# Kernel optimization log

Hardware: AMD Instinct MI355X
Metric: run time of the kernel (lower is better)

## Reference

```python
import jax, jax.numpy as jnp
import numpy as np

B, NPG, K_DYN, H, C = 8, 4096, 8, 2, 64   # graphs, nodes/graph, kNN, heads, head dim
N = B * NPG
E = 524288
CAP = 20.0
NEG = 0.2


def _leaky(x):
    return jax.nn.leaky_relu(x, NEG)


def _bn(x, g, b):
    # BatchNorm1d, training-mode statistics over the node dim (biased var, eps=1e-5)
    m = jnp.mean(x, 0)
    v = jnp.mean((x - m) ** 2, 0)
    return (x - m) * jax.lax.rsqrt(v + 1e-5) * g + b


def _gatv2(x, src, dst, wl, bl, wr, br, att, bias, ea=None, we=None):
    # PyG GATv2Conv, heads=H, concat=False (mean over heads), dropout in eval mode
    n = x.shape[0]
    xl = (x @ wl + bl).reshape(n, H, C)   # source transform
    xr = (x @ wr + br).reshape(n, H, C)   # target transform
    e = xl[src] + xr[dst]                 # [E,H,C]
    if ea is not None:
        e = e + (ea @ we).reshape(-1, H, C)
    e = _leaky(e)
    logit = jnp.sum(e * att, -1)          # [E,H]
    m = jax.ops.segment_max(logit, dst, num_segments=n)
    m = jnp.where(jnp.isfinite(m), m, 0.0)
    ex = jnp.exp(logit - m[dst])
    den = jax.ops.segment_sum(ex, dst, num_segments=n) + 1e-16
    alpha = ex / den[dst]                 # segment softmax over incoming edges
    out = jax.ops.segment_sum(alpha[..., None] * xl[src], dst, num_segments=n)
    return jnp.mean(out, 1) + bias        # concat=False -> mean over heads


def _dyn_agg(h, w1, b1, w2, b2):
    # dynamic kNN in feature space (per graph, detached), gather-MLP-mean aggregation
    h3 = h.reshape(B, NPG, -1)
    hd = jax.lax.stop_gradient(h3)
    sq = jnp.sum(hd * hd, -1)
    d = sq[:, :, None] + sq[:, None, :] - 2.0 * jnp.einsum('bnd,bmd->bnm', hd, hd)
    d = jnp.where(jnp.eye(NPG, dtype=bool), jnp.inf, d)  # exclude self
    _, idx = jax.lax.top_k(-d, K_DYN)                    # [B,n,K] nearest neighbors
    hn = jax.vmap(lambda hb, ib: hb[ib])(h3, idx)        # [B,n,K,D]
    hi = jnp.broadcast_to(h3[:, :, None, :], hn.shape)
    msg = jnp.concatenate([hi, hn - hi], -1)             # cat([h[row], h[col]-h[row]])
    msg = _leaky(msg @ w1 + b1) @ w2 + b2
    # every node emits exactly K edges -> scatter_add/count == mean over K
    return jnp.mean(msg, 2).reshape(N, -1)


def setup_inputs():
    key = jax.random.key(0)
    ks = iter(jax.random.split(key, 64))
    def rn(shape, scale=1.0):
        return jax.random.normal(next(ks), shape, dtype=jnp.float32) * scale
    hd = 64
    return {
        'x': rn((N, 5)),
        'edge_attr': rn((E, 6)),
        'edge_index': jax.random.randint(next(ks), (2, E), 0, N, dtype=jnp.int32),
        'g1_wl': rn((5, H * C), 0.3), 'g1_bl': rn((H * C,), 0.02),
        'g1_wr': rn((5, H * C), 0.3), 'g1_br': rn((H * C,), 0.02),
        'g1_we': rn((6, H * C), 0.3),
        'g1_att': rn((H, C), 0.1), 'g1_bias': rn((C,), 0.02),
        'bn1_g': jnp.ones((hd,), jnp.float32), 'bn1_b': jnp.zeros((hd,), jnp.float32),
        'em_w1': rn((2 * hd, hd), 0.08), 'em_b1': rn((hd,), 0.02),
        'em_w2': rn((hd, hd), 0.12), 'em_b2': rn((hd,), 0.02),
        'bn2_g': jnp.ones((hd,), jnp.float32), 'bn2_b': jnp.zeros((hd,), jnp.float32),
        'g2_wl': rn((hd, H * C), 0.12), 'g2_bl': rn((H * C,), 0.02),
        'g2_wr': rn((hd, H * C), 0.12), 'g2_br': rn((H * C,), 0.02),
        'g2_att': rn((H, C), 0.1), 'g2_bias': rn((C,), 0.02),
        'bn3_g': jnp.ones((hd,), jnp.float32), 'bn3_b': jnp.zeros((hd,), jnp.float32),
        'gate_w1': rn((hd, hd), 0.12), 'gate_b1': rn((hd,), 0.02),
        'gate_w2': rn((hd, 1), 0.12), 'gate_b2': rn((1,), 0.02),
        'ctx_w1': rn((hd, hd), 0.12), 'ctx_b1': rn((hd,), 0.02),
        'ctx_w2': rn((hd, hd), 0.12), 'ctx_b2': rn((hd,), 0.02),
        'dec_w1': rn((hd + hd + 5, 128), 0.09), 'dec_b1': rn((128,), 0.02),
        'ln_g': jnp.ones((128,), jnp.float32), 'ln_b': jnp.zeros((128,), jnp.float32),
        'dec_w2': rn((128, 64), 0.09), 'dec_b2': rn((64,), 0.02),
        'dec_w3': rn((64, 3), 0.12), 'dec_b3': rn((3,), 0.02),
    }


def reference(x, edge_attr, edge_index, g1_wl, g1_bl, g1_wr, g1_br, g1_we, g1_att, g1_bias,
              bn1_g, bn1_b, em_w1, em_b1, em_w2, em_b2, bn2_g, bn2_b,
              g2_wl, g2_bl, g2_wr, g2_br, g2_att, g2_bias, bn3_g, bn3_b,
              gate_w1, gate_b1, gate_w2, gate_b2, ctx_w1, ctx_b1, ctx_w2, ctx_b2,
              dec_w1, dec_b1, ln_g, ln_b, dec_w2, dec_b2, dec_w3, dec_b3):
    src, dst = edge_index[0], edge_index[1]
    h = _leaky(_bn(_gatv2(x, src, dst, g1_wl, g1_bl, g1_wr, g1_br, g1_att, g1_bias, edge_attr, g1_we), bn1_g, bn1_b))
    h = _leaky(_bn(_dyn_agg(h, em_w1, em_b1, em_w2, em_b2), bn2_g, bn2_b))
    h = _leaky(_bn(_gatv2(h, src, dst, g2_wl, g2_bl, g2_wr, g2_br, g2_att, g2_bias), bn3_g, bn3_b))
    # attentional pooling per graph (equal-sized graphs -> reshape instead of segment ops)
    h3 = h.reshape(B, NPG, -1)
    gate = jnp.tanh(h3 @ gate_w1 + gate_b1) @ gate_w2 + gate_b2   # [B,n,1]
    alpha = jax.nn.softmax(gate, axis=1)
    g = jnp.sum(alpha * h3, 1)                                    # [B,hd]
    g = _leaky(g @ ctx_w1 + ctx_b1) @ ctx_w2 + ctx_b2
    gfull = jnp.broadcast_to(g[:, None, :], (B, NPG, g.shape[-1])).reshape(N, -1)
    hf = jnp.concatenate([h, gfull, x], 1)                        # [N,133]
    d1 = _leaky(hf @ dec_w1 + dec_b1)
    mu = jnp.mean(d1, -1, keepdims=True)
    var = jnp.mean((d1 - mu) ** 2, -1, keepdims=True)
    d1 = (d1 - mu) * jax.lax.rsqrt(var + 1e-5) * ln_g + ln_b       # LayerNorm(128)
    d2 = _leaky(d1 @ dec_w2 + dec_b2)
    out3 = d2 @ dec_w3 + dec_b3
    return x[:, :3] + jnp.tanh(out3) * CAP
```

## Files before the change

### kernel.cpp

```cpp
#include <hip/hip_runtime.h>

#define NN   32768
#define NPG  4096
#define NGR  8
#define NE   524288
#define NEGS 0.2f

typedef float  v4f __attribute__((ext_vector_type(4)));
typedef short  v8s __attribute__((ext_vector_type(8)));

__device__ __forceinline__ float lrelu(float x){ return x > 0.f ? x : NEGS*x; }

__device__ __forceinline__ unsigned short f2bf(float v){
  unsigned int u = __float_as_uint(v);
  u = u + 0x7fffu + ((u >> 16) & 1u);
  return (unsigned short)(u >> 16);
}
__device__ __forceinline__ float bf2f(unsigned short s){
  return __uint_as_float(((unsigned int)s) << 16);
}

__global__ __launch_bounds__(256) void k_xform5(
    const float* __restrict__ x,
    const float* __restrict__ wl, const float* __restrict__ bl,
    const float* __restrict__ wr, const float* __restrict__ br,
    float* __restrict__ xl, float* __restrict__ xr) {
  int t = blockIdx.x * 256 + threadIdx.x;
  int n = t >> 7, oc = t & 127;
  const float* xp = x + n * 5;
  float a = bl[oc], b = br[oc];
  #pragma unroll
  for (int j = 0; j < 5; ++j) {
    float v = xp[j];
    a += v * wl[j * 128 + oc];
    b += v * wr[j * 128 + oc];
  }
  xl[t] = a; xr[t] = b;
}

__global__ __launch_bounds__(256) void k_count(const int* __restrict__ dst, int* __restrict__ cnt) {
  int e = blockIdx.x * 256 + threadIdx.x;
  atomicAdd(&cnt[dst[e]], 1);
}

__global__ __launch_bounds__(1024) void k_scan(const int* __restrict__ cnt,
                                               int* __restrict__ start, int* __restrict__ cur) {
  __shared__ int sh[1024];
  int t = threadIdx.x;
  int base = t * 32;
  int s = 0;
  for (int i = 0; i < 32; ++i) s += cnt[base + i];
  sh[t] = s;
  __syncthreads();
  for (int ofs = 1; ofs < 1024; ofs <<= 1) {
    int v = (t >= ofs) ? sh[t - ofs] : 0;
    __syncthreads();
    sh[t] += v;
    __syncthreads();
  }
  int run = sh[t] - s;
  for (int i = 0; i < 32; ++i) {
    start[base + i] = run; cur[base + i] = run;
    run += cnt[base + i];
  }
}

__global__ __launch_bounds__(256) void k_scatter(const int* __restrict__ dst,
                                                 const int* __restrict__ srcv,
                                                 int* __restrict__ cur,
                                                 int* __restrict__ bkt_e, int* __restrict__ bkt_s) {
  int e = blockIdx.x * 256 + threadIdx.x;
  int p = atomicAdd(&cur[dst[e]], 1);
  bkt_e[p] = e;
  bkt_s[p] = srcv[e];
}

template<int HAS_EA>
__global__ __launch_bounds__(256) void k_gat_edge(
    const float* __restrict__ xl, const float* __restrict__ xr,
    const float* __restrict__ ea,
    const float* __restrict__ we, const float* __restrict__ att,
    const float* __restrict__ bias,
    const int* __restrict__ start, const int* __restrict__ cnt,
    const int* __restrict__ bsrc, const int* __restrict__ bedge,
    float* __restrict__ out) {
  int wv = threadIdx.x >> 6, lane = threadIdx.x & 63;
  int n = blockIdx.x * 4 + wv;
  int s0 = start[n], deg = cnt[n];
  float xr0 = xr[n * 128 + lane], xr1 = xr[n * 128 + 64 + lane];
  float a0 = att[lane], a1 = att[64 + lane];
  float w0r[6], w1r[6];
  if (HAS_EA) {
    #pragma unroll
    for (int j = 0; j < 6; ++j) { w0r[j] = we[j * 128 + lane]; w1r[j] = we[j * 128 + 64 + lane]; }
  }
  float m0 = -1e30f, m1 = -1e30f, d0 = 0.f, d1 = 0.f, o0 = 0.f, o1 = 0.f;

  float l0 = 0.f, l1 = 0.f, ecur[6], enxt[6];
  int sNxt = 0;
  if (deg > 0) {
    int sCur = bsrc[s0];
    l0 = xl[sCur * 128 + lane]; l1 = xl[sCur * 128 + 64 + lane];
    if (HAS_EA) {
      int e = bedge[s0];
      #pragma unroll
      for (int j = 0; j < 6; ++j) ecur[j] = ea[e * 6 + j];
    }
    if (deg > 1) sNxt = bsrc[s0 + 1];
  }

  for (int i = 0; i < deg; ++i) {
    float l0c = l0, l1c = l1;
    if (i + 1 < deg) {
      l0 = xl[sNxt * 128 + lane]; l1 = xl[sNxt * 128 + 64 + lane];
      if (HAS_EA) {
        int e = bedge[s0 + i + 1];
        #pragma unroll
        for (int j = 0; j < 6; ++j) enxt[j] = ea[e * 6 + j];
      }
    }
    int sNN = (i + 2 < deg) ? bsrc[s0 + i + 2] : 0;

    float e0 = l0c + xr0, e1 = l1c + xr1;
    if (HAS_EA) {
      float p0 = 0.f, p1 = 0.f;
      #pragma unroll
      for (int j = 0; j < 6; ++j) { p0 += ecur[j] * w0r[j]; p1 += ecur[j] * w1r[j]; }
      e0 += p0; e1 += p1;
      #pragma unroll
      for (int j = 0; j < 6; ++j) ecur[j] = enxt[j];
    }
    e0 = lrelu(e0); e1 = lrelu(e1);
    float t0 = e0 * a0, t1 = e1 * a1;
    #pragma unroll
    for (int d = 32; d > 0; d >>= 1) { t0 += __shfl_xor(t0, d, 64); t1 += __shfl_xor(t1, d, 64); }
    if (t0 > m0) { float r = __expf(m0 - t0); o0 *= r; d0 *= r; m0 = t0; }
    float p0e = __expf(t0 - m0); d0 += p0e; o0 += p0e * l0c;
    if (t1 > m1) { float r = __expf(m1 - t1); o1 *= r; d1 *= r; m1 = t1; }
    float p1e = __expf(t1 - m1); d1 += p1e; o1 += p1e * l1c;
    sNxt = sNN;
  }
  float r0 = o0 / (d0 + 1e-16f);
  float r1 = o1 / (d1 + 1e-16f);
  out[n * 64 + lane] = 0.5f * (r0 + r1) + bias[lane];
}

__global__ __launch_bounds__(256) void k_bn_reduce(const float* __restrict__ h, float* __restrict__ stat) {
  float s = 0.f, s2 = 0.f;
  for (int i = blockIdx.x * 256 + threadIdx.x; i < NN * 64; i += gridDim.x * 256) {
    float v = h[i]; s += v; s2 += v * v;
  }
  __shared__ float sh[512];
  sh[threadIdx.x] = s; sh[256 + threadIdx.x] = s2;
  __syncthreads();
  if (threadIdx.x < 64) {
    int c = threadIdx.x;
    float a = sh[c] + sh[c + 64] + sh[c + 128] + sh[c + 192];
    float b = sh[256 + c] + sh[256 + c + 64] + sh[256 + c + 128] + sh[256 + c + 192];
    atomicAdd(&stat[c], a);
    atomicAdd(&stat[64 + c], b);
  }
}

__global__ void k_bn_final(const float* __restrict__ stat, const float* __restrict__ g,
                           const float* __restrict__ b, float* __restrict__ AB) {
  int c = threadIdx.x;
  float mean = stat[c] * (1.f / NN);
  float var  = stat[64 + c] * (1.f / NN) - mean * mean;
  float rstd = rsqrtf(var + 1e-5f);
  float A = g[c] * rstd;
  AB[c] = A; AB[64 + c] = b[c] - mean * A;
}

__global__ __launch_bounds__(256) void k_bn_apply(float* __restrict__ h, const float* __restrict__ AB) {
  int i = blockIdx.x * 256 + threadIdx.x;
  int c = i & 63;
  h[i] = lrelu(h[i] * AB[c] + AB[64 + c]);
}

__global__ __launch_bounds__(256) void k_split_sq(const float* __restrict__ h,
    unsigned short* __restrict__ hi, unsigned short* __restrict__ lo, float* __restrict__ sq) {
  int wv = threadIdx.x >> 6, lane = threadIdx.x & 63;
  int n = blockIdx.x * 4 + wv;
  int b = n >> 12, npg = n & (NPG - 1);
  float v = h[n * 64 + lane];
  unsigned short hu = f2bf(v);
  float hf = bf2f(hu);
  int idx = ((b * 8 + (lane >> 3)) * NPG + npg) * 8 + (lane & 7);
  hi[idx] = hu;
  lo[idx] = f2bf(v - hf);
  float s = v * v;
  #pragma unroll
  for (int d = 32; d > 0; d >>= 1) s += __shfl_xor(s, d, 64);
  if (lane == 0) sq[n] = s;
}

__global__ __launch_bounds__(256) void k_gram_topk(
    const unsigned short* __restrict__ hbhi, const unsigned short* __restrict__ hblo,
    const float* __restrict__ sq, int* __restrict__ cand) {
  __shared__ alignas(16) unsigned short Ahi[8 * 64 * 8], Alo[8 * 64 * 8];
  __shared__ alignas(16) unsigned short Bhi[2 * 8 * 64 * 8];
  __shared__ alignas(16) unsigned short Blo[2 * 8 * 64 * 8];
  __shared__ float sqch[2][64];

  int tid = threadIdx.x, wv = tid >> 6, lane = tid & 63;
  int b = blockIdx.x & 7, rblk = blockIdx.x >> 3;
  int gbase = b * NPG, rowbase = gbase + rblk * 64;
  int l15 = lane & 15, l4 = lane >> 4;

  #pragma unroll
  for (int r = 0; r < 2; ++r) {
    int chn = tid + r * 256;
    int s = chn >> 6, row = chn & 63;
    int gi = ((b * 8 + s) * NPG + rblk * 64 + row) * 8;
    *(uint4*)&Ahi[chn * 8] = *(const uint4*)&hbhi[gi];
    *(uint4*)&Alo[chn * 8] = *(const uint4*)&hblo[gi];
  }
  #pragma unroll
  for (int r = 0; r < 2; ++r) {
    int chn = tid + r * 256;
    int s = chn >> 6, node = chn & 63;
    int gi = ((b * 8 + s) * NPG + node) * 8;
    *(uint4*)&Bhi[chn * 8] = *(const uint4*)&hbhi[gi];
    *(uint4*)&Blo[chn * 8] = *(const uint4*)&hblo[gi];
  }
  if (tid < 64) sqch[0][tid] = 0.5f * sq[gbase + tid];
  __syncthreads();

  int rloc = wv * 16 + l15;
  int rnode = rowbase + rloc;
  v8s ofh[2], ofl[2];
  #pragma unroll
  for (int ks = 0; ks < 2; ++ks) {
    int s = ks * 4 + l4;
    ofh[ks] = *(v8s*)&Ahi[(s * 64 + rloc) * 8];
    ofl[ks] = *(v8s*)&Alo[(s * 64 + rloc) * 8];
  }

  float td[10]; int ti[10];
  #pragma unroll
  for (int j = 0; j < 10; ++j) { td[j] = 1e30f; ti[j] = 0x7fffffff; }

  int cur = 0;
  for (int it = 0; it < NPG / 64; ++it) {
    bool more = (it + 1 < NPG / 64);
    uint4 nh0, nh1, nl0, nl1;
    float nsq = 0.f;
    if (more) {
      int tb = (it + 1) * 64;
      int s0 = tid >> 6, n0 = tid & 63;
      int chn1 = tid + 256, s1 = chn1 >> 6, n1 = chn1 & 63;
      int g0 = ((b * 8 + s0) * NPG + tb + n0) * 8;
      int g1 = ((b * 8 + s1) * NPG + tb + n1) * 8;
      nh0 = *(const uint4*)&hbhi[g0];
      nh1 = *(const uint4*)&hbhi[g1];
      nl0 = *(const uint4*)&hblo[g0];
      nl1 = *(const uint4*)&hblo[g1];
      if (tid < 64) nsq = 0.5f * sq[gbase + tb + tid];
    }

    int base = cur * 512;
    int cb = gbase + it * 64;
    #pragma unroll
    for (int cg = 0; cg < 4; ++cg) {
      v8s ch0 = *(v8s*)&Bhi[(base + (0 + l4) * 64 + cg * 16 + l15) * 8];
      v8s ch1 = *(v8s*)&Bhi[(base + (4 + l4) * 64 + cg * 16 + l15) * 8];
      v8s cl0 = *(v8s*)&Blo[(base + (0 + l4) * 64 + cg * 16 + l15) * 8];
      v8s cl1 = *(v8s*)&Blo[(base + (4 + l4) * 64 + cg * 16 + l15) * 8];
      v4f accA = {0.f, 0.f, 0.f, 0.f}, accB = {0.f, 0.f, 0.f, 0.f};
      accA = __builtin_amdgcn_mfma_f32_16x16x32_bf16(ch0, ofh[0], accA, 0, 0, 0);
      accB = __builtin_amdgcn_mfma_f32_16x16x32_bf16(ch0, ofl[0], accB, 0, 0, 0);
      accA = __builtin_amdgcn_mfma_f32_16x16x32_bf16(ch1, ofh[1], accA, 0, 0, 0);
      accB = __builtin_amdgcn_mfma_f32_16x16x32_bf16(ch1, ofl[1], accB, 0, 0, 0);
      accB = __builtin_amdgcn_mfma_f32_16x16x32_bf16(cl0, ofh[0], accB, 0, 0, 0);
      accB = __builtin_amdgcn_mfma_f32_16x16x32_bf16(cl1, ofh[1], accB, 0, 0, 0);
      int kb = cg * 16 + l4 * 4;
      float k0 = sqch[cur][kb + 0] - (accA[0] + accB[0]);
      float k1 = sqch[cur][kb + 1] - (accA[1] + accB[1]);
      float k2 = sqch[cur][kb + 2] - (accA[2] + accB[2]);
      float k3 = sqch[cur][kb + 3] - (accA[3] + accB[3]);
      float gmin = fminf(fminf(k0, k1), fminf(k2, k3));
      if (gmin < td[9]) {
        float kk[4] = {k0, k1, k2, k3};
        #pragma unroll
        for (int r = 0; r < 4; ++r) {
          if (kk[r] < td[9]) {
            float cd = kk[r]; int ci = cb + kb + r;
            #pragma unroll
            for (int u = 0; u < 10; ++u) {
              bool bt = cd < td[u];
              float nd = bt ? cd : td[u]; int nc = bt ? ci : ti[u];
              float od = bt ? td[u] : cd; int oc = bt ? ti[u] : ci;
              td[u] = nd; ti[u] = nc; cd = od; ci = oc;
            }
          }
        }
      }
    }

    if (more) {
      int nb_ = (cur ^ 1) * 4096;
      *(uint4*)&Bhi[nb_ + tid * 8]         = nh0;
      *(uint4*)&Bhi[nb_ + (tid + 256) * 8] = nh1;
      *(uint4*)&Blo[nb_ + tid * 8]         = nl0;
      *(uint4*)&Blo[nb_ + (tid + 256) * 8] = nl1;
      if (tid < 64) sqch[cur ^ 1][tid] = nsq;
    }
    __syncthreads();
    cur ^= 1;
  }

  float* mbd = (float*)Bhi;
  int*   mbi = (int*)Blo;
  #pragma unroll
  for (int j = 0; j < 10; ++j) {
    mbd[(rloc * 4 + l4) * 10 + j] = td[j];
    mbi[(rloc * 4 + l4) * 10 + j] = ti[j];
  }
  __syncthreads();
  if (tid < 64) {
    int rn = rowbase + tid;
    float fd[12]; int fi[12];
    #pragma unroll
    for (int j = 0; j < 12; ++j) { fd[j] = 1e30f; fi[j] = 0x7fffffff; }
    #pragma unroll 1
    for (int u = 0; u < 40; ++u) {
      float cd = mbd[tid * 40 + u];
      int   ci = mbi[tid * 40 + u];
      if (ci != rn && (cd < fd[11] || (cd == fd[11] && ci < fi[11]))) {
        #pragma unroll
        for (int v = 0; v < 12; ++v) {
          bool better = (cd < fd[v]) || (cd == fd[v] && ci < fi[v]);
          if (better) { float tf = fd[v]; int tq = fi[v]; fd[v] = cd; fi[v] = ci; cd = tf; ci = tq; }
        }
      }
    }
    #pragma unroll
    for (int j = 0; j < 12; ++j) cand[rn * 12 + j] = fi[j];
  }
}

__global__ __launch_bounds__(256) void k_refine(
    const float* __restrict__ h, const int* __restrict__ cand, int* __restrict__ knn) {
  int wv = threadIdx.x >> 6, lane = threadIdx.x & 63;
  int n = blockIdx.x * 4 + wv;
  float hn = h[n * 64 + lane];
  float td[8]; int ti[8];
  #pragma unroll
  for (int j = 0; j < 8; ++j) { td[j] = 1e30f; ti[j] = 0x7fffffff; }
  #pragma unroll 1
  for (int j = 0; j < 12; ++j) {
    int c = cand[n * 12 + j];
    float df = h[c * 64 + lane] - hn;
    float s = df * df;
    #pragma unroll
    for (int d = 32; d > 0; d >>= 1) s += __shfl_xor(s, d, 64);
    if (s < td[7] || (s == td[7] && c < ti[7])) {
      float cd = s; int ci = c;
      #pragma unroll
      for (int u = 0; u < 8; ++u) {
        bool better = (cd < td[u]) || (cd == td[u] && ci < ti[u]);
        if (better) { float tf = td[u]; int tq = ti[u]; td[u] = cd; ti[u] = ci; cd = tf; ci = tq; }
      }
    }
  }
  #pragma unroll
  for (int u = 0; u < 8; ++u) {
    if (lane == u) knn[n * 8 + u] = ti[u];
  }
}

__global__ __launch_bounds__(256) void k_dynmlp(
    const float* __restrict__ h, const int* __restrict__ knn,
    const float* __restrict__ w1, const float* __restrict__ b1,
    const float* __restrict__ w2, const float* __restrict__ b2,
    float* __restrict__ out) {
  __shared__ alignas(16) float smem[128 * 64];
  __shared__ float outacc[8 * 64];
  int t = threadIdx.x;
  int nb = blockIdx.x * 8;
  for (int u = t; u < 512; u += 256) outacc[u] = 0.f;

  int p = t & 63;
  int n = nb + (p >> 3);
  int m = knn[n * 8 + (p & 7)];
  for (int qq = (t >> 6); qq < 32; qq += 4) {
    int j0 = qq * 4;
    float4 v;
    if (j0 < 64) {
      v = *(const float4*)(h + n * 64 + j0);
    } else {
      float4 a = *(const float4*)(h + m * 64 + (j0 - 64));
      float4 c = *(const float4*)(h + n * 64 + (j0 - 64));
      v.x = a.x - c.x; v.y = a.y - c.y; v.z = a.z - c.z; v.w = a.w - c.w;
    }
    smem[(j0 + 0) * 64 + p] = v.x;
    smem[(j0 + 1) * 64 + p] = v.y;
    smem[(j0 + 2) * 64 + p] = v.z;
    smem[(j0 + 3) * 64 + p] = v.w;
  }
  __syncthreads();

  int pq = t >> 4, cq = t & 15;
  float acc[4][4];
  #pragma unroll
  for (int c = 0; c < 4; ++c) {
    float bv = b1[cq * 4 + c];
    #pragma unroll
    for (int i = 0; i < 4; ++i) acc[i][c] = bv;
  }
  for (int j = 0; j < 128; ++j) {
    float4 av = *(float4*)&smem[j * 64 + pq * 4];
    float4 wv = *(const float4*)&w1[j * 64 + cq * 4];
    float aa[4] = {av.x, av.y, av.z, av.w};
    float ww[4] = {wv.x, wv.y, wv.z, wv.w};
    #pragma unroll
    for (int i = 0; i < 4; ++i)
      #pragma unroll
      for (int c = 0; c < 4; ++c) acc[i][c] += aa[i] * ww[c];
  }
  __syncthreads();
  #pragma unroll
  for (int c = 0; c < 4; ++c)
    #pragma unroll
    for (int i = 0; i < 4; ++i)
      smem[(cq * 4 + c) * 68 + pq * 4 + i] = lrelu(acc[i][c]);
  __syncthreads();

  float a2[4][4];
  #pragma unroll
  for (int i = 0; i < 4; ++i)
    #pragma unroll
    for (int c = 0; c < 4; ++c) a2[i][c] = 0.f;
  for (int j = 0; j < 64; ++j) {
    float4 av = *(float4*)&smem[j * 68 + pq * 4];
    float4 wv = *(const float4*)&w2[j * 64 + cq * 4];
    float aa[4] = {av.x, av.y, av.z, av.w};
    float ww[4] = {wv.x, wv.y, wv.z, wv.w};
    #pragma unroll
    for (int i = 0; i < 4; ++i)
      #pragma unroll
      for (int c = 0; c < 4; ++c) a2[i][c] += aa[i] * ww[c];
  }
  #pragma unroll
  for (int i = 0; i < 4; ++i) {
    int nloc = (pq * 4 + i) >> 3;
    #pragma unroll
    for (int c = 0; c < 4; ++c) atomicAdd(&outacc[nloc * 64 + cq * 4 + c], a2[i][c]);
  }
  __syncthreads();
  for (int u = t; u < 512; u += 256) {
    out[(nb + (u >> 6)) * 64 + (u & 63)] = outacc[u] * 0.125f + b2[u & 63];
  }
}

__global__ __launch_bounds__(256) void k_xform64(
    const float* __restrict__ h,
    const float* __restrict__ wl, const float* __restrict__ bl,
    const float* __restrict__ wr, const float* __restrict__ br,
    float* __restrict__ xl, float* __restrict__ xr) {
  __shared__ alignas(16) float hT[64 * 20];
  int t = threadIdx.x;
  int nb = blockIdx.x * 16;
  {
    int n = t >> 4, qj = t & 15;
    float4 v = *(const float4*)(h + (nb + n) * 64 + qj * 4);
    hT[(qj * 4 + 0) * 20 + n] = v.x;
    hT[(qj * 4 + 1) * 20 + n] = v.y;
    hT[(qj * 4 + 2) * 20 + n] = v.z;
    hT[(qj * 4 + 3) * 20 + n] = v.w;
  }
  __syncthreads();
  int pq = t >> 6, cq = t & 63;
  int oc = cq * 4;
  const float* wb; const float* bb; float* ob; int ocl;
  if (oc < 128) { wb = wl + oc;         bb = bl + oc;         ob = xl; ocl = oc; }
  else          { wb = wr + (oc - 128); bb = br + (oc - 128); ob = xr; ocl = oc - 128; }
  float acc[4][4];
  #pragma unroll
  for (int c = 0; c < 4; ++c) {
    float bv = bb[c];
    #pragma unroll
    for (int i = 0; i < 4; ++i) acc[i][c] = bv;
  }
  for (int j = 0; j < 64; ++j) {
    float4 av = *(float4*)&hT[j * 20 + pq * 4];
    float4 wv = *(const float4*)(wb + j * 128);
    float aa[4] = {av.x, av.y, av.z, av.w};
    float ww[4] = {wv.x, wv.y, wv.z, wv.w};
    #pragma unroll
    for (int i = 0; i < 4; ++i)
      #pragma unroll
      for (int c = 0; c < 4; ++c) acc[i][c] += aa[i] * ww[c];
  }
  #pragma unroll
  for (int i = 0; i < 4; ++i) {
    int n = nb + pq * 4 + i;
    #pragma unroll
    for (int c = 0; c < 4; ++c) ob[n * 128 + ocl + c] = acc[i][c];
  }
}

__global__ __launch_bounds__(256) void k_gate(
    const float* __restrict__ h3, const float* __restrict__ w1, const float* __restrict__ b1,
    const float* __restrict__ w2, const float* __restrict__ b2, float* __restrict__ gates) {
  __shared__ float hsh[4][64];
  int wv = threadIdx.x >> 6, lane = threadIdx.x & 63;
  int n = blockIdx.x * 4 + wv;
  hsh[wv][lane] = h3[n * 64 + lane];
  __syncthreads();
  float s = b1[lane];
  for (int j = 0; j < 64; ++j) s += hsh[wv][j] * w1[j * 64 + lane];
  float tv = tanhf(s) * w2[lane];
  #pragma unroll
  for (int d = 32; d > 0; d >>= 1) tv += __shfl_xor(tv, d, 64);
  if (lane == 0) gates[n] = tv + b2[0];
}

__global__ __launch_bounds__(1024) void k_pool(
    const float* __restrict__ gates, const float* __restrict__ h3,
    float* __restrict__ pexp, float* __restrict__ gpool) {
  int b = blockIdx.x, t = threadIdx.x;
  const float* g = gates + b * NPG;
  __shared__ float red[1024];
  float m = -1e30f;
  for (int i = t; i < NPG; i += 1024) m = fmaxf(m, g[i]);
  red[t] = m; __syncthreads();
  for (int s = 512; s > 0; s >>= 1) { if (t < s) red[t] = fmaxf(red[t], red[t + s]); __syncthreads(); }
  m = red[0]; __syncthreads();
  float sum = 0.f;
  for (int i = t; i < NPG; i += 1024) { float p = __expf(g[i] - m); pexp[b * NPG + i] = p; sum += p; }
  red[t] = sum; __syncthreads();
  for (int s = 512; s > 0; s >>= 1) { if (t < s) red[t] += red[t + s]; __syncthreads(); }
  float den = red[0];
  __syncthreads();
  int grp = t >> 6, c = t & 63;
  float acc = 0.f;
  for (int i = grp; i < NPG; i += 16) acc += pexp[b * NPG + i] * h3[(b * NPG + i) * 64 + c];
  red[t] = acc; __syncthreads();
  if (t < 64) {
    float a = 0.f;
    for (int qq = 0; qq < 16; ++qq) a += red[qq * 64 + t];
    gpool[b * 64 + t] = a / den;
  }
}

__global__ void k_ctx(const float* __restrict__ gpool,
                      const float* __restrict__ w1, const float* __restrict__ b1,
                      const float* __restrict__ w2, const float* __restrict__ b2,
                      float* __restrict__ gctx) {
  __shared__ float gsh[64], tsh[64];
  int b = blockIdx.x, c = threadIdx.x;
  gsh[c] = gpool[b * 64 + c];
  __syncthreads();
  float s = b1[c];
  for (int j = 0; j < 64; ++j) s += gsh[j] * w1[j * 64 + c];
  tsh[c] = lrelu(s);
  __syncthreads();
  float o = b2[c];
  for (int j = 0; j < 64; ++j) o += tsh[j] * w2[j * 64 + c];
  gctx[b * 64 + c] = o;
}

__global__ __launch_bounds__(128) void k_decoder(
    const float* __restrict__ h3, const float* __restrict__ gctx, const float* __restrict__ x,
    const float* __restrict__ w1, const float* __restrict__ b1,
    const float* __restrict__ lng, const float* __restrict__ lnb,
    const float* __restrict__ w2, const float* __restrict__ b2,
    const float* __restrict__ w3, const float* __restrict__ b3,
    float* __restrict__ out) {
  __shared__ alignas(16) float hf[16 * 136];
  __shared__ alignas(16) float dT[16 * 132];
  __shared__ float d2[16 * 65];
  __shared__ float mu[16], rs[16];
  int t = threadIdx.x;
  int nb = blockIdx.x * 16;
  int gb = nb >> 12;
  for (int u = t; u < 16 * 64; u += 128) { int p = u >> 6, j = u & 63; hf[p * 136 + j] = h3[(nb + p) * 64 + j]; }
  for (int u = t; u < 16 * 64; u += 128) { int p = u >> 6, j = u & 63; hf[p * 136 + 64 + j] = gctx[gb * 64 + j]; }
  for (int u = t; u < 16 * 5; u += 128) { int p = u / 5, j = u % 5; hf[p * 136 + 128 + j] = x[(nb + p) * 5 + j]; }
  __syncthreads();
  float acc[16];
  #pragma unroll
  for (int p = 0; p < 16; ++p) acc[p] = b1[t];
  for (int j4 = 0; j4 < 128; j4 += 4) {
    float w0 = w1[(j4 + 0) * 128 + t], wv1 = w1[(j4 + 1) * 128 + t];
    float wv2 = w1[(j4 + 2) * 128 + t], wv3 = w1[(j4 + 3) * 128 + t];
    #pragma unroll
    for (int p = 0; p < 16; ++p) {
      float4 hv = *(float4*)&hf[p * 136 + j4];
      acc[p] += hv.x * w0 + hv.y * wv1 + hv.z * wv2 + hv.w * wv3;
    }
  }
  for (int j = 128; j < 133; ++j) {
    float w = w1[j * 128 + t];
    #pragma unroll
    for (int p = 0; p < 16; ++p) acc[p] += hf[p * 136 + j] * w;
  }
  #pragma unroll
  for (int p = 0; p < 16; ++p) dT[p * 132 + t] = lrelu(acc[p]);
  __syncthreads();
  if (t < 16) {
    float s = 0.f, s2 = 0.f;
    for (int j = 0; j < 128; ++j) { float v = dT[t * 132 + j]; s += v; s2 += v * v; }
    float mn = s * (1.f / 128.f);
    float vr = s2 * (1.f / 128.f) - mn * mn;
    mu[t] = mn; rs[t] = rsqrtf(vr + 1e-5f);
  }
  __syncthreads();
  float lg = lng[t], lb = lnb[t];
  #pragma unroll
  for (int p = 0; p < 16; ++p) dT[p * 132 + t] = (dT[p * 132 + t] - mu[p]) * rs[p] * lg + lb;
  __syncthreads();
  if (t < 64) {
    float a2[16];
    #pragma unroll
    for (int p = 0; p < 16; ++p) a2[p] = b2[t];
    for (int j4 = 0; j4 < 128; j4 += 4) {
      float w0 = w2[(j4 + 0) * 64 + t], wv1 = w2[(j4 + 1) * 64 + t];
      float wv2 = w2[(j4 + 2) * 64 + t], wv3 = w2[(j4 + 3) * 64 + t];
      #pragma unroll
      for (int p = 0; p < 16; ++p) {
        float4 dv = *(float4*)&dT[p * 132 + j4];
        a2[p] += dv.x * w0 + dv.y * wv1 + dv.z * wv2 + dv.w * wv3;
      }
    }
    #pragma unroll
    for (int p = 0; p < 16; ++p) d2[p * 65 + t] = lrelu(a2[p]);
  }
  __syncthreads();
  if (t < 48) {
    int p = t / 3, k = t % 3;
    float o = b3[k];
    for (int j = 0; j < 64; ++j) o += d2[p * 65 + j] * w3[j * 3 + k];
    out[(nb + p) * 3 + k] = x[(nb + p) * 5 + k] + tanhf(o) * 20.0f;
  }
}

#define O_XL     0ul
#define O_HBHI   0ul
#define O_HBLO   4194304ul
#define O_SQ     8388608ul
#define O_KNN    8519680ul
#define O_XR     16777216ul
#define O_CAND   16777216ul
#define O_H1     33554432ul
#define O_H2     41943040ul
#define O_CNT    50331648ul
#define O_START  50462720ul
#define O_CUR    50593792ul
#define O_BKT    50724864ul
#define O_BSRC   52822016ul
#define O_STAT   54919168ul
#define O_AB     54919680ul
#define O_GATES  54920192ul
#define O_PEXP   55051264ul
#define O_GPOOL  55182336ul
#define O_GCTX   55184384ul

extern "C" void kernel_launch(void* const* d_in, const int* in_sizes, int n_in,
                              void* d_out, int out_size, void* d_ws, size_t ws_size,
                              hipStream_t stream) {
  (void)in_sizes; (void)n_in; (void)out_size; (void)ws_size;
  const float* x      = (const float*)d_in[0];
  const float* eattr  = (const float*)d_in[1];
  const int*   ei     = (const int*)d_in[2];
  const float* g1_wl  = (const float*)d_in[3];
  const float* g1_bl  = (const float*)d_in[4];
  const float* g1_wr  = (const float*)d_in[5];
  const float* g1_br  = (const float*)d_in[6];
  const float* g1_we  = (const float*)d_in[7];
  const float* g1_att = (const float*)d_in[8];
  const float* g1_bias= (const float*)d_in[9];
  const float* bn1_g  = (const float*)d_in[10];
  const float* bn1_b  = (const float*)d_in[11];
  const float* em_w1  = (const float*)d_in[12];
  const float* em_b1  = (const float*)d_in[13];
  const float* em_w2  = (const float*)d_in[14];
  const float* em_b2  = (const float*)d_in[15];
  const float* bn2_g  = (const float*)d_in[16];
  const float* bn2_b  = (const float*)d_in[17];
  const float* g2_wl  = (const float*)d_in[18];
  const float* g2_bl  = (const float*)d_in[19];
  const float* g2_wr  = (const float*)d_in[20];
  const float* g2_br  = (const float*)d_in[21];
  const float* g2_att = (const float*)d_in[22];
  const float* g2_bias= (const float*)d_in[23];
  const float* bn3_g  = (const float*)d_in[24];
  const float* bn3_b  = (const float*)d_in[25];
  const float* gt_w1  = (const float*)d_in[26];
  const float* gt_b1  = (const float*)d_in[27];
  const float* gt_w2  = (const float*)d_in[28];
  const float* gt_b2  = (const float*)d_in[29];
  const float* cx_w1  = (const float*)d_in[30];
  const float* cx_b1  = (const float*)d_in[31];
  const float* cx_w2  = (const float*)d_in[32];
  const float* cx_b2  = (const float*)d_in[33];
  const float* dc_w1  = (const float*)d_in[34];
  const float* dc_b1  = (const float*)d_in[35];
  const float* ln_g   = (const float*)d_in[36];
  const float* ln_b   = (const float*)d_in[37];
  const float* dc_w2  = (const float*)d_in[38];
  const float* dc_b2  = (const float*)d_in[39];
  const float* dc_w3  = (const float*)d_in[40];
  const float* dc_b3  = (const float*)d_in[41];

  char* ws = (char*)d_ws;
  float* xl    = (float*)(ws + O_XL);
  float* xr    = (float*)(ws + O_XR);
  float* h1    = (float*)(ws + O_H1);
  float* h2    = (float*)(ws + O_H2);
  int*   cnt   = (int*)(ws + O_CNT);
  int*   start = (int*)(ws + O_START);
  int*   cur   = (int*)(ws + O_CUR);
  int*   bkt   = (int*)(ws + O_BKT);
  int*   bsrc  = (int*)(ws + O_BSRC);
  unsigned short* hbhi = (unsigned short*)(ws + O_HBHI);
  unsigned short* hblo = (unsigned short*)(ws + O_HBLO);
  float* sq    = (float*)(ws + O_SQ);
  int*   knn   = (int*)(ws + O_KNN);
  int*   cand  = (int*)(ws + O_CAND);
  float* stat  = (float*)(ws + O_STAT);
  float* AB    = (float*)(ws + O_AB);
  float* gates = (float*)(ws + O_GATES);
  float* pexp  = (float*)(ws + O_PEXP);
  float* gpool = (float*)(ws + O_GPOOL);
  float* gctx  = (float*)(ws + O_GCTX);

  const int* src = ei;
  const int* dst = ei + NE;

  hipMemsetAsync(cnt, 0, NN * 4, stream);
  k_xform5<<<NN * 128 / 256, 256, 0, stream>>>(x, g1_wl, g1_bl, g1_wr, g1_br, xl, xr);
  k_count<<<NE / 256, 256, 0, stream>>>(dst, cnt);
  k_scan<<<1, 1024, 0, stream>>>(cnt, start, cur);
  k_scatter<<<NE / 256, 256, 0, stream>>>(dst, src, cur, bkt, bsrc);
  k_gat_edge<1><<<NN / 4, 256, 0, stream>>>(xl, xr, eattr, g1_we, g1_att, g1_bias,
                                            start, cnt, bsrc, bkt, h1);
  hipMemsetAsync(stat, 0, 512, stream);
  k_bn_reduce<<<256, 256, 0, stream>>>(h1, stat);
  k_bn_final<<<1, 64, 0, stream>>>(stat, bn1_g, bn1_b, AB);
  k_bn_apply<<<NN * 64 / 256, 256, 0, stream>>>(h1, AB);

  k_split_sq<<<NN / 4, 256, 0, stream>>>(h1, hbhi, hblo, sq);
  k_gram_topk<<<NGR * (NPG / 64), 256, 0, stream>>>(hbhi, hblo, sq, cand);
  k_refine<<<NN / 4, 256, 0, stream>>>(h1, cand, knn);
  k_dynmlp<<<NN / 8, 256, 0, stream>>>(h1, knn, em_w1, em_b1, em_w2, em_b2, h2);
  hipMemsetAsync(stat, 0, 512, stream);
  k_bn_reduce<<<256, 256, 0, stream>>>(h2, stat);
  k_bn_final<<<1, 64, 0, stream>>>(stat, bn2_g, bn2_b, AB);
  k_bn_apply<<<NN * 64 / 256, 256, 0, stream>>>(h2, AB);

  k_xform64<<<NN / 16, 256, 0, stream>>>(h2, g2_wl, g2_bl, g2_wr, g2_br, xl, xr);
  k_gat_edge<0><<<NN / 4, 256, 0, stream>>>(xl, xr, nullptr, nullptr, g2_att, g2_bias,
                                            start, cnt, bsrc, bkt, h1);
  hipMemsetAsync(stat, 0, 512, stream);
  k_bn_reduce<<<256, 256, 0, stream>>>(h1, stat);
  k_bn_final<<<1, 64, 0, stream>>>(stat, bn3_g, bn3_b, AB);
  k_bn_apply<<<NN * 64 / 256, 256, 0, stream>>>(h1, AB);

  k_gate<<<NN / 4, 256, 0, stream>>>(h1, gt_w1, gt_b1, gt_w2, gt_b2, gates);
  k_pool<<<NGR, 1024, 0, stream>>>(gates, h1, pexp, gpool);
  k_ctx<<<NGR, 64, 0, stream>>>(gpool, cx_w1, cx_b1, cx_w2, cx_b2, gctx);

  k_decoder<<<NN / 16, 128, 0, stream>>>(h1, gctx, x, dc_w1, dc_b1, ln_g, ln_b,
                                         dc_w2, dc_b2, dc_w3, dc_b3, (float*)d_out);
}
```

Measured before the change: 1.160 ms.

## Factor dynamic edge MLP first layer per node and unroll GAT edge loop

Splits the edge MLP's first linear layer into per-node projections A=h@W1a+b1 and C=h@W1b. The per-edge work then becomes lrelu(A_n-C_n+C_m), averaged over the 8 neighbours, and the second layer is applied once per node because the mean commutes with the linear map. This removes the per-edge 128x64 and 64x64 matmuls at the cost of an extra kernel and intermediate buffers reusing workspace. The GAT edge loop also processes two edges per iteration to raise memory-level parallelism, at the cost of more registers.

```diff
diff --git a/kernel.cpp b/kernel.cpp
--- a/kernel.cpp
+++ b/kernel.cpp
@@ -96,50 +96,87 @@
   }
   float m0 = -1e30f, m1 = -1e30f, d0 = 0.f, d1 = 0.f, o0 = 0.f, o1 = 0.f;
 
-  float l0 = 0.f, l1 = 0.f, ecur[6], enxt[6];
-  int sNxt = 0;
-  if (deg > 0) {
-    int sCur = bsrc[s0];
-    l0 = xl[sCur * 128 + lane]; l1 = xl[sCur * 128 + 64 + lane];
+  int np = deg >> 1;
+  float A0 = 0.f, A1 = 0.f, B0 = 0.f, B1 = 0.f;
+  float NA0 = 0.f, NA1 = 0.f, NB0 = 0.f, NB1 = 0.f;
+  float EA[6], EB[6], NEA[6], NEB[6];
+  if (np > 0) {
+    int sa = bsrc[s0], sb = bsrc[s0 + 1];
+    A0 = xl[sa * 128 + lane]; A1 = xl[sa * 128 + 64 + lane];
+    B0 = xl[sb * 128 + lane]; B1 = xl[sb * 128 + 64 + lane];
     if (HAS_EA) {
-      int e = bedge[s0];
+      int eai = bedge[s0], ebi = bedge[s0 + 1];
       #pragma unroll
-      for (int j = 0; j < 6; ++j) ecur[j] = ea[e * 6 + j];
-    }
-    if (deg > 1) sNxt = bsrc[s0 + 1];
-  }
-
-  for (int i = 0; i < deg; ++i) {
-    float l0c = l0, l1c = l1;
-    if (i + 1 < deg) {
-      l0 = xl[sNxt * 128 + lane]; l1 = xl[sNxt * 128 + 64 + lane];
+      for (int j = 0; j < 6; ++j) { EA[j] = ea[eai * 6 + j]; EB[j] = ea[ebi * 6 + j]; }
+    }
+  }
+
+  for (int p = 0; p < np; ++p) {
+    if (p + 1 < np) {
+      int i2 = s0 + 2 * (p + 1);
+      int sa = bsrc[i2], sb = bsrc[i2 + 1];
+      NA0 = xl[sa * 128 + lane]; NA1 = xl[sa * 128 + 64 + lane];
+      NB0 = xl[sb * 128 + lane]; NB1 = xl[sb * 128 + 64 + lane];
       if (HAS_EA) {
-        int e = bedge[s0 + i + 1];
+        int eai = bedge[i2], ebi = bedge[i2 + 1];
         #pragma unroll
-        for (int j = 0; j < 6; ++j) enxt[j] = ea[e * 6 + j];
+        for (int j = 0; j < 6; ++j) { NEA[j] = ea[eai * 6 + j]; NEB[j] = ea[ebi * 6 + j]; }
       }
     }
-    int sNN = (i + 2 < deg) ? bsrc[s0 + i + 2] : 0;
-
-    float e0 = l0c + xr0, e1 = l1c + xr1;
+    float e0a = A0 + xr0, e1a = A1 + xr1, e0b = B0 + xr0, e1b = B1 + xr1;
     if (HAS_EA) {
+      float pa0 = 0.f, pa1 = 0.f, pb0 = 0.f, pb1 = 0.f;
+      #pragma unroll
+      for (int j = 0; j < 6; ++j) {
+        pa0 += EA[j] * w0r[j]; pa1 += EA[j] * w1r[j];
+        pb0 += EB[j] * w0r[j]; pb1 += EB[j] * w1r[j];
+      }
+      e0a += pa0; e1a += pa1; e0b += pb0; e1b += pb1;
+    }
+    e0a = lrelu(e0a); e1a = lrelu(e1a); e0b = lrelu(e0b); e1b = lrelu(e1b);
+    float ta0 = e0a * a0, ta1 = e1a * a1, tb0 = e0b * a0, tb1 = e1b * a1;
+    #pragma unroll
+    for (int d = 32; d > 0; d >>= 1) {
+      ta0 += __shfl_xor(ta0, d, 64); ta1 += __shfl_xor(ta1, d, 64);
+      tb0 += __shfl_xor(tb0, d, 64); tb1 += __shfl_xor(tb1, d, 64);
+    }
+    float tm0 = fmaxf(ta0, tb0);
+    if (tm0 > m0) { float r = __expf(m0 - tm0); o0 *= r; d0 *= r; m0 = tm0; }
+    float pa = __expf(ta0 - m0), pb = __expf(tb0 - m0);
+    d0 += pa + pb; o0 += pa * A0 + pb * B0;
+    float tm1 = fmaxf(ta1, tb1);
+    if (tm1 > m1) { float r = __expf(m1 - tm1); o1 *= r; d1 *= r; m1 = tm1; }
+    float qa = __expf(ta1 - m1), qb = __expf(tb1 - m1);
+    d1 += qa + qb; o1 += qa * A1 + qb * B1;
+    A0 = NA0; A1 = NA1; B0 = NB0; B1 = NB1;
+    if (HAS_EA) {
+      #pragma unroll
+      for (int j = 0; j < 6; ++j) { EA[j] = NEA[j]; EB[j] = NEB[j]; }
+    }
+  }
+
+  if (deg & 1) {
+    int i = s0 + deg - 1;
+    int s = bsrc[i];
+    float l0 = xl[s * 128 + lane], l1 = xl[s * 128 + 64 + lane];
+    float e0 = l0 + xr0, e1 = l1 + xr1;
+    if (HAS_EA) {
+      int e = bedge[i];
       float p0 = 0.f, p1 = 0.f;
       #pragma unroll
-      for (int j = 0; j < 6; ++j) { p0 += ecur[j] * w0r[j]; p1 += ecur[j] * w1r[j]; }
+      for (int j = 0; j < 6; ++j) { float v = ea[e * 6 + j]; p0 += v * w0r[j]; p1 += v * w1r[j]; }
       e0 += p0; e1 += p1;
-      #pragma unroll
-      for (int j = 0; j < 6; ++j) ecur[j] = enxt[j];
     }
     e0 = lrelu(e0); e1 = lrelu(e1);
     float t0 = e0 * a0, t1 = e1 * a1;
     #pragma unroll
     for (int d = 32; d > 0; d >>= 1) { t0 += __shfl_xor(t0, d, 64); t1 += __shfl_xor(t1, d, 64); }
     if (t0 > m0) { float r = __expf(m0 - t0); o0 *= r; d0 *= r; m0 = t0; }
-    float p0e = __expf(t0 - m0); d0 += p0e; o0 += p0e * l0c;
+    float p0e = __expf(t0 - m0); d0 += p0e; o0 += p0e * l0;
     if (t1 > m1) { float r = __expf(m1 - t1); o1 *= r; d1 *= r; m1 = t1; }
-    float p1e = __expf(t1 - m1); d1 += p1e; o1 += p1e * l1c;
-    sNxt = sNN;
-  }
+    float p1e = __expf(t1 - m1); d1 += p1e; o1 += p1e * l1;
+  }
+
   float r0 = o0 / (d0 + 1e-16f);
   float r1 = o1 / (d1 + 1e-16f);
   out[n * 64 + lane] = 0.5f * (r0 + r1) + bias[lane];
@@ -370,88 +407,77 @@
   }
 }
 
-__global__ __launch_bounds__(256) void k_dynmlp(
-    const float* __restrict__ h, const int* __restrict__ knn,
+__global__ __launch_bounds__(256) void k_dynprep(
+    const float* __restrict__ h,
     const float* __restrict__ w1, const float* __restrict__ b1,
-    const float* __restrict__ w2, const float* __restrict__ b2,
-    float* __restrict__ out) {
-  __shared__ alignas(16) float smem[128 * 64];
-  __shared__ float outacc[8 * 64];
+    float* __restrict__ A, float* __restrict__ C) {
+  __shared__ alignas(16) float hT[64 * 20];
   int t = threadIdx.x;
-  int nb = blockIdx.x * 8;
-  for (int u = t; u < 512; u += 256) outacc[u] = 0.f;
-
-  int p = t & 63;
-  int n = nb + (p >> 3);
-  int m = knn[n * 8 + (p & 7)];
-  for (int qq = (t >> 6); qq < 32; qq += 4) {
-    int j0 = qq * 4;
-    float4 v;
-    if (j0 < 64) {
-      v = *(const float4*)(h + n * 64 + j0);
-    } else {
-      float4 a = *(const float4*)(h + m * 64 + (j0 - 64));
-      float4 c = *(const float4*)(h + n * 64 + (j0 - 64));
-      v.x = a.x - c.x; v.y = a.y - c.y; v.z = a.z - c.z; v.w = a.w - c.w;
-    }
-    smem[(j0 + 0) * 64 + p] = v.x;
-    smem[(j0 + 1) * 64 + p] = v.y;
-    smem[(j0 + 2) * 64 + p] = v.z;
-    smem[(j0 + 3) * 64 + p] = v.w;
-  }
-  __syncthreads();
-
-  int pq = t >> 4, cq = t & 15;
-  float acc[4][4];
-  #pragma unroll
-  for (int c = 0; c < 4; ++c) {
-    float bv = b1[cq * 4 + c];
-    #pragma unroll
-    for (int i = 0; i < 4; ++i) acc[i][c] = bv;
-  }
-  for (int j = 0; j < 128; ++j) {
-    float4 av = *(float4*)&smem[j * 64 + pq * 4];
-    float4 wv = *(const float4*)&w1[j * 64 + cq * 4];
-    float aa[4] = {av.x, av.y, av.z, av.w};
-    float ww[4] = {wv.x, wv.y, wv.z, wv.w};
-    #pragma unroll
-    for (int i = 0; i < 4; ++i)
-      #pragma unroll
-      for (int c = 0; c < 4; ++c) acc[i][c] += aa[i] * ww[c];
-  }
-  __syncthreads();
-  #pragma unroll
-  for (int c = 0; c < 4; ++c)
-    #pragma unroll
-    for (int i = 0; i < 4; ++i)
-      smem[(cq * 4 + c) * 68 + pq * 4 + i] = lrelu(acc[i][c]);
-  __syncthreads();
-
-  float a2[4][4];
-  #pragma unroll
-  for (int i = 0; i < 4; ++i)
-    #pragma unroll
-    for (int c = 0; c < 4; ++c) a2[i][c] = 0.f;
+  int nb = blockIdx.x * 16;
+  {
+    int n = t >> 4, qj = t & 15;
+    float4 v = *(const float4*)(h + (nb + n) * 64 + qj * 4);
+    hT[(qj * 4 + 0) * 20 + n] = v.x;
+    hT[(qj * 4 + 1) * 20 + n] = v.y;
+    hT[(qj * 4 + 2) * 20 + n] = v.z;
+    hT[(qj * 4 + 3) * 20 + n] = v.w;
+  }
+  __syncthreads();
+  int pq = t >> 6, cq = t & 63;
+  int oc = cq * 2;
+  const float* wb; float* ob; int ocl; float bv0, bv1;
+  if (oc < 64) { wb = w1 + oc;             ob = A; ocl = oc;      bv0 = b1[oc]; bv1 = b1[oc + 1]; }
+  else         { wb = w1 + 4096 + (oc-64); ob = C; ocl = oc - 64; bv0 = 0.f;    bv1 = 0.f; }
+  float acc[4][2];
+  #pragma unroll
+  for (int i = 0; i < 4; ++i) { acc[i][0] = bv0; acc[i][1] = bv1; }
   for (int j = 0; j < 64; ++j) {
-    float4 av = *(float4*)&smem[j * 68 + pq * 4];
-    float4 wv = *(const float4*)&w2[j * 64 + cq * 4];
-    float aa[4] = {av.x, av.y, av.z, av.w};
-    float ww[4] = {wv.x, wv.y, wv.z, wv.w};
-    #pragma unroll
-    for (int i = 0; i < 4; ++i)
-      #pragma unroll
-      for (int c = 0; c < 4; ++c) a2[i][c] += aa[i] * ww[c];
+    float4 av = *(float4*)&hT[j * 20 + pq * 4];
+    float2 wv = *(const float2*)(wb + j * 64);
+    acc[0][0] += av.x * wv.x; acc[0][1] += av.x * wv.y;
+    acc[1][0] += av.y * wv.x; acc[1][1] += av.y * wv.y;
+    acc[2][0] += av.z * wv.x; acc[2][1] += av.z * wv.y;
+    acc[3][0] += av.w * wv.x; acc[3][1] += av.w * wv.y;
   }
   #pragma unroll
   for (int i = 0; i < 4; ++i) {
-    int nloc = (pq * 4 + i) >> 3;
-    #pragma unroll
-    for (int c = 0; c < 4; ++c) atomicAdd(&outacc[nloc * 64 + cq * 4 + c], a2[i][c]);
-  }
-  __syncthreads();
-  for (int u = t; u < 512; u += 256) {
-    out[(nb + (u >> 6)) * 64 + (u & 63)] = outacc[u] * 0.125f + b2[u & 63];
-  }
+    int n = nb + pq * 4 + i;
+    ob[n * 64 + ocl]     = acc[i][0];
+    ob[n * 64 + ocl + 1] = acc[i][1];
+  }
+}
+
+__global__ __launch_bounds__(256) void k_dynagg(
+    const float* __restrict__ A, const float* __restrict__ C,
+    const int* __restrict__ knn, const float* __restrict__ w2,
+    const float* __restrict__ b2, float* __restrict__ out) {
+  __shared__ float w2sh[64 * 64];
+  __shared__ float ysh[4 * 64];
+  int t = threadIdx.x, wv = t >> 6, lane = t & 63;
+  int n = blockIdx.x * 4 + wv;
+  for (int u = t; u < 1024; u += 256) *(float4*)&w2sh[u * 4] = *(const float4*)&w2[u * 4];
+  float a  = A[n * 64 + lane];
+  float cn = C[n * 64 + lane];
+  int mm[8];
+  #pragma unroll
+  for (int k = 0; k < 8; ++k) mm[k] = knn[n * 8 + k];
+  float cm[8];
+  #pragma unroll
+  for (int k = 0; k < 8; ++k) cm[k] = C[mm[k] * 64 + lane];
+  float bse = a - cn;
+  float s = 0.f;
+  #pragma unroll
+  for (int k = 0; k < 8; ++k) s += lrelu(bse + cm[k]);
+  ysh[wv * 64 + lane] = s * 0.125f;
+  __syncthreads();
+  float acc = b2[lane];
+  for (int j = 0; j < 64; j += 4) {
+    float y0 = ysh[wv * 64 + j],     y1 = ysh[wv * 64 + j + 1];
+    float y2 = ysh[wv * 64 + j + 2], y3 = ysh[wv * 64 + j + 3];
+    acc += y0 * w2sh[j * 64 + lane]       + y1 * w2sh[(j + 1) * 64 + lane]
+         + y2 * w2sh[(j + 2) * 64 + lane] + y3 * w2sh[(j + 3) * 64 + lane];
+  }
+  out[n * 64 + lane] = acc;
 }
 
 __global__ __launch_bounds__(256) void k_xform64(
@@ -639,11 +665,13 @@
 
 #define O_XL     0ul
 #define O_HBHI   0ul
+#define O_A      0ul
 #define O_HBLO   4194304ul
 #define O_SQ     8388608ul
 #define O_KNN    8519680ul
 #define O_XR     16777216ul
 #define O_CAND   16777216ul
+#define O_C      16777216ul
 #define O_H1     33554432ul
 #define O_H2     41943040ul
 #define O_CNT    50331648ul
@@ -720,6 +748,8 @@
   float* sq    = (float*)(ws + O_SQ);
   int*   knn   = (int*)(ws + O_KNN);
   int*   cand  = (int*)(ws + O_CAND);
+  float* Aar   = (float*)(ws + O_A);
+  float* Car   = (float*)(ws + O_C);
   float* stat  = (float*)(ws + O_STAT);
   float* AB    = (float*)(ws + O_AB);
   float* gates = (float*)(ws + O_GATES);
@@ -745,7 +775,8 @@
   k_split_sq<<<NN / 4, 256, 0, stream>>>(h1, hbhi, hblo, sq);
   k_gram_topk<<<NGR * (NPG / 64), 256, 0, stream>>>(hbhi, hblo, sq, cand);
   k_refine<<<NN / 4, 256, 0, stream>>>(h1, cand, knn);
-  k_dynmlp<<<NN / 8, 256, 0, stream>>>(h1, knn, em_w1, em_b1, em_w2, em_b2, h2);
+  k_dynprep<<<NN / 16, 256, 0, stream>>>(h1, em_w1, em_b1, Aar, Car);
+  k_dynagg<<<NN / 4, 256, 0, stream>>>(Aar, Car, knn, em_w2, em_b2, h2);
   hipMemsetAsync(stat, 0, 512, stream);
   k_bn_reduce<<<256, 256, 0, stream>>>(h2, stat);
   k_bn_final<<<1, 64, 0, stream>>>(stat, bn2_g, bn2_b, AB);
```

New measurement: 1.028 ms. 11.4% less time.
